# Kernel tuning notes

Hardware: AMD Instinct MI355X
Metric: run time of the kernel (lower is better)

Reference implementation:

```python
import jax, jax.numpy as jnp
import numpy as np

LAMBDA_LAME = 1.0
MU_LAME = 0.5
JACOBIAN_WEIGHT = 0.1
ERROR_BOUND = 0.01


def setup_inputs() -> dict:
    key = jax.random.key(0)
    df = jax.random.normal(key, (2, 3, 192, 192, 192), dtype=jnp.float32)
    return {"deformation_field": df}


def _grad(x, axis):
    # matches torch.gradient / np.gradient (edge_order=1): central diff in the
    # interior, one-sided first-order at the boundaries, unit spacing.
    return jnp.gradient(x, axis=axis)


def _robust(x, delta):
    abs_x = jnp.abs(x)
    return jnp.where(abs_x <= delta, 0.5 * x * x, delta * (abs_x - 0.5 * delta))


def reference(deformation_field):
    u = deformation_field[:, 0]  # [B, D, H, W]
    v = deformation_field[:, 1]
    w = deformation_field[:, 2]

    du_dx, du_dy, du_dz = _grad(u, 1), _grad(u, 2), _grad(u, 3)
    dv_dx, dv_dy, dv_dz = _grad(v, 1), _grad(v, 2), _grad(v, 3)
    dw_dx, dw_dy, dw_dz = _grad(w, 1), _grad(w, 2), _grad(w, 3)

    E_xx, E_yy, E_zz = du_dx, dv_dy, dw_dz
    E_xy = 0.5 * (du_dy + dv_dx)
    E_xz = 0.5 * (du_dz + dw_dx)
    E_yz = 0.5 * (dv_dz + dw_dy)
    trace_E = E_xx + E_yy + E_zz

    d = ERROR_BOUND
    tr_l = _robust(trace_E, d)
    energy = (0.5 * LAMBDA_LAME * tr_l ** 2
              + MU_LAME * (_robust(E_xx, d) ** 2 + _robust(E_yy, d) ** 2
                           + _robust(E_zz, d) ** 2
                           + 2.0 * (_robust(E_xy, d) ** 2
                                    + _robust(E_xz, d) ** 2
                                    + _robust(E_yz, d) ** 2)))

    jac = ((1 + du_dx) * ((1 + dv_dy) * (1 + dw_dz) - dv_dz * dw_dy)
           - du_dy * (dv_dx * (1 + dw_dz) - dv_dz * (1 + dw_dx))
           + du_dz * (dv_dx * dw_dy - (1 + dv_dy) * (1 + dw_dx)))
    jac_penalty = jax.nn.relu(-jac)

    total = jnp.mean(energy) + JACOBIAN_WEIGHT * jnp.mean(jac_penalty)
    return total
```

## Files before the change

kernel.cpp:

```cpp
#include <hip/hip_runtime.h>

#define DIM 192
#define PLANE (DIM * DIM)
#define VOL ((size_t)PLANE * DIM)
#define NTOT (2.0 * 14155776.0 / 2.0)

__device__ __forceinline__ float robustf(float x) {
    float ax = fabsf(x);
    return (ax <= 0.01f) ? (0.5f * x * x) : (0.01f * (ax - 0.005f));
}

__device__ __forceinline__ float4 ldg4(const float* __restrict__ p) {
    return *(const float4*)p;
}

__device__ __forceinline__ float voxel_loss(
    float du_dx, float du_dy, float du_dz,
    float dv_dx, float dv_dy, float dv_dz,
    float dw_dx, float dw_dy, float dw_dz) {
    const float E_xy = 0.5f * (du_dy + dv_dx);
    const float E_xz = 0.5f * (du_dz + dw_dx);
    const float E_yz = 0.5f * (dv_dz + dw_dy);
    const float tr   = du_dx + dv_dy + dw_dz;

    const float rtr = robustf(tr);
    const float rxx = robustf(du_dx), ryy = robustf(dv_dy), rzz = robustf(dw_dz);
    const float rxy = robustf(E_xy),  rxz = robustf(E_xz),  ryz = robustf(E_yz);

    const float energy = 0.5f * rtr * rtr
                       + 0.5f * (rxx * rxx + ryy * ryy + rzz * rzz
                                 + 2.0f * (rxy * rxy + rxz * rxz + ryz * ryz));

    const float jac =
          (1.0f + du_dx) * ((1.0f + dv_dy) * (1.0f + dw_dz) - dv_dz * dw_dy)
        - du_dy * (dv_dx * (1.0f + dw_dz) - dv_dz * (1.0f + dw_dx))
        + du_dz * (dv_dx * dw_dy - (1.0f + dv_dy) * (1.0f + dw_dx));

    return energy + 0.1f * fmaxf(-jac, 0.0f);
}

__device__ __forceinline__ float4 zgrad(float4 c, float lf, float rt,
                                        bool leftEdge, bool rightEdge) {
    float4 g;
    g.x = leftEdge  ? (c.y - c.x) : 0.5f * (c.y - lf);
    g.y = 0.5f * (c.z - c.x);
    g.z = 0.5f * (c.w - c.y);
    g.w = rightEdge ? (c.w - c.z) : 0.5f * (rt - c.z);
    return g;
}

__global__ __launch_bounds__(256)
void elastic_main(const float* __restrict__ df, double* __restrict__ acc) {
    const int tx = threadIdx.x;
    const int ty = threadIdx.y;
    const int k4 = tx * 4;
    const int j  = blockIdx.x * 4 + ty;
    const int i0 = blockIdx.y * 16;
    const int b  = blockIdx.z;

    const float* __restrict__ u = df + (size_t)(b * 3 + 0) * VOL;
    const float* __restrict__ v = df + (size_t)(b * 3 + 1) * VOL;
    const float* __restrict__ w = df + (size_t)(b * 3 + 2) * VOL;

    const int jp = (j < DIM - 1) ? j + 1 : j;
    const int jm = (j > 0) ? j - 1 : j;
    const float sy = ((jp - jm) == 2) ? 0.5f : 1.0f;

    const bool act = (tx < 48);
    const bool leftEdge  = (tx == 0);
    const bool rightEdge = (tx == 47);

    float vsum = 0.0f;

    for (int ii = 0; ii < 16; ++ii) {
        const int i = i0 + ii;
        const int ip = (i < DIM - 1) ? i + 1 : i;
        const int im = (i > 0) ? i - 1 : i;
        const float sx = ((ip - im) == 2) ? 0.5f : 1.0f;

        const size_t oC  = (size_t)i  * PLANE + (size_t)j  * DIM + k4;
        const size_t oXp = (size_t)ip * PLANE + (size_t)j  * DIM + k4;
        const size_t oXm = (size_t)im * PLANE + (size_t)j  * DIM + k4;
        const size_t oYp = (size_t)i  * PLANE + (size_t)jp * DIM + k4;
        const size_t oYm = (size_t)i  * PLANE + (size_t)jm * DIM + k4;

        float4 uc, vc, wc;
        float4 uxp, uxm, vxp, vxm, wxp, wxm;
        float4 uyp, uym, vyp, vym, wyp, wym;

        if (act) {
            uc  = ldg4(u + oC);  vc  = ldg4(v + oC);  wc  = ldg4(w + oC);
            uxp = ldg4(u + oXp); uxm = ldg4(u + oXm);
            vxp = ldg4(v + oXp); vxm = ldg4(v + oXm);
            wxp = ldg4(w + oXp); wxm = ldg4(w + oXm);
            uyp = ldg4(u + oYp); uym = ldg4(u + oYm);
            vyp = ldg4(v + oYp); vym = ldg4(v + oYm);
            wyp = ldg4(w + oYp); wym = ldg4(w + oYm);
        } else {
            uc = vc = wc = make_float4(0.f, 0.f, 0.f, 0.f);
        }

        const float ulf = __shfl_up(uc.w, 1);
        const float vlf = __shfl_up(vc.w, 1);
        const float wlf = __shfl_up(wc.w, 1);
        const float urt = __shfl_down(uc.x, 1);
        const float vrt = __shfl_down(vc.x, 1);
        const float wrt = __shfl_down(wc.x, 1);

        if (act) {
            const float4 du_dz = zgrad(uc, ulf, urt, leftEdge, rightEdge);
            const float4 dv_dz = zgrad(vc, vlf, vrt, leftEdge, rightEdge);
            const float4 dw_dz = zgrad(wc, wlf, wrt, leftEdge, rightEdge);

            float4 du_dx, dv_dx, dw_dx, du_dy, dv_dy, dw_dy;
            du_dx.x = (uxp.x - uxm.x) * sx; du_dx.y = (uxp.y - uxm.y) * sx;
            du_dx.z = (uxp.z - uxm.z) * sx; du_dx.w = (uxp.w - uxm.w) * sx;
            dv_dx.x = (vxp.x - vxm.x) * sx; dv_dx.y = (vxp.y - vxm.y) * sx;
            dv_dx.z = (vxp.z - vxm.z) * sx; dv_dx.w = (vxp.w - vxm.w) * sx;
            dw_dx.x = (wxp.x - wxm.x) * sx; dw_dx.y = (wxp.y - wxm.y) * sx;
            dw_dx.z = (wxp.z - wxm.z) * sx; dw_dx.w = (wxp.w - wxm.w) * sx;
            du_dy.x = (uyp.x - uym.x) * sy; du_dy.y = (uyp.y - uym.y) * sy;
            du_dy.z = (uyp.z - uym.z) * sy; du_dy.w = (uyp.w - uym.w) * sy;
            dv_dy.x = (vyp.x - vym.x) * sy; dv_dy.y = (vyp.y - vym.y) * sy;
            dv_dy.z = (vyp.z - vym.z) * sy; dv_dy.w = (vyp.w - vym.w) * sy;
            dw_dy.x = (wyp.x - wym.x) * sy; dw_dy.y = (wyp.y - wym.y) * sy;
            dw_dy.z = (wyp.z - wym.z) * sy; dw_dy.w = (wyp.w - wym.w) * sy;

            vsum += voxel_loss(du_dx.x, du_dy.x, du_dz.x,
                               dv_dx.x, dv_dy.x, dv_dz.x,
                               dw_dx.x, dw_dy.x, dw_dz.x);
            vsum += voxel_loss(du_dx.y, du_dy.y, du_dz.y,
                               dv_dx.y, dv_dy.y, dv_dz.y,
                               dw_dx.y, dw_dy.y, dw_dz.y);
            vsum += voxel_loss(du_dx.z, du_dy.z, du_dz.z,
                               dv_dx.z, dv_dy.z, dv_dz.z,
                               dw_dx.z, dw_dy.z, dw_dz.z);
            vsum += voxel_loss(du_dx.w, du_dy.w, du_dz.w,
                               dv_dx.w, dv_dy.w, dv_dz.w,
                               dw_dx.w, dw_dy.w, dw_dz.w);
        }
    }

    #pragma unroll
    for (int off = 32; off > 0; off >>= 1)
        vsum += __shfl_down(vsum, off, 64);

    __shared__ float wpart[4];
    if (tx == 0) wpart[ty] = vsum;
    __syncthreads();
    if (tx == 0 && ty == 0) {
        double s = (double)wpart[0] + (double)wpart[1]
                 + (double)wpart[2] + (double)wpart[3];
        unsafeAtomicAdd(acc, s);
    }
}

__global__ void elastic_finalize(const double* __restrict__ acc, float* __restrict__ out) {
    out[0] = (float)(acc[0] * (1.0 / 14155776.0));
}

extern "C" void kernel_launch(void* const* d_in, const int* in_sizes, int n_in,
                              void* d_out, int out_size, void* d_ws, size_t ws_size,
                              hipStream_t stream) {
    const float* df = (const float*)d_in[0];
    double* acc = (double*)d_ws;
    float* out = (float*)d_out;

    hipMemsetAsync(d_ws, 0, sizeof(double), stream);

    dim3 grid(48, 12, 2);
    dim3 block(64, 4);
    elastic_main<<<grid, block, 0, stream>>>(df, acc);
    elastic_finalize<<<1, 1, 0, stream>>>(acc, out);
}
```

Measured before the change: 261.4 us.

## Reuse x-neighbor planes via a rolling register window and lengthen the x-chunk

Each thread now keeps the previous and current x-planes of u, v and w in registers and rotates them every step. Per iteration it loads only the next x-plane plus the y-neighbours, cutting global/cache loads from 15 to 9 float4s. The x-chunk per block grows from 16 to 24 planes, which cuts the grid to 768 blocks, and a min-blocks hint is added to launch_bounds. The longer chunk amortises the warm-up loads but lowers the total number of resident waves, which may reduce latency hiding.

```diff
diff --git a/kernel.cpp b/kernel.cpp
--- a/kernel.cpp
+++ b/kernel.cpp
@@ -3,7 +3,6 @@
 #define DIM 192
 #define PLANE (DIM * DIM)
 #define VOL ((size_t)PLANE * DIM)
-#define NTOT (2.0 * 14155776.0 / 2.0)
 
 __device__ __forceinline__ float robustf(float x) {
     float ax = fabsf(x);
@@ -12,6 +11,11 @@
 
 __device__ __forceinline__ float4 ldg4(const float* __restrict__ p) {
     return *(const float4*)p;
+}
+
+__device__ __forceinline__ float4 sub_scale(float4 a, float4 b, float s) {
+    return make_float4((a.x - b.x) * s, (a.y - b.y) * s,
+                       (a.z - b.z) * s, (a.w - b.w) * s);
 }
 
 __device__ __forceinline__ float voxel_loss(
@@ -49,13 +53,13 @@
     return g;
 }
 
-__global__ __launch_bounds__(256)
+__global__ __launch_bounds__(256, 4)
 void elastic_main(const float* __restrict__ df, double* __restrict__ acc) {
     const int tx = threadIdx.x;
     const int ty = threadIdx.y;
     const int k4 = tx * 4;
     const int j  = blockIdx.x * 4 + ty;
-    const int i0 = blockIdx.y * 16;
+    const int i0 = blockIdx.y * 24;
     const int b  = blockIdx.z;
 
     const float* __restrict__ u = df + (size_t)(b * 3 + 0) * VOL;
@@ -70,34 +74,38 @@
     const bool leftEdge  = (tx == 0);
     const bool rightEdge = (tx == 47);
 
+    float4 um, vm, wm, uc, vc, wc;
+    um = vm = wm = uc = vc = wc = make_float4(0.f, 0.f, 0.f, 0.f);
+
+    {
+        const int im1 = (i0 > 0) ? i0 - 1 : 0;
+        const size_t oM = (size_t)im1 * PLANE + (size_t)j * DIM + k4;
+        const size_t oC = (size_t)i0  * PLANE + (size_t)j * DIM + k4;
+        if (act) {
+            um = ldg4(u + oM); vm = ldg4(v + oM); wm = ldg4(w + oM);
+            uc = ldg4(u + oC); vc = ldg4(v + oC); wc = ldg4(w + oC);
+        }
+    }
+
     float vsum = 0.0f;
 
-    for (int ii = 0; ii < 16; ++ii) {
-        const int i = i0 + ii;
-        const int ip = (i < DIM - 1) ? i + 1 : i;
-        const int im = (i > 0) ? i - 1 : i;
-        const float sx = ((ip - im) == 2) ? 0.5f : 1.0f;
+    for (int ii = 0; ii < 24; ++ii) {
+        const int i   = i0 + ii;
+        const int ip1 = (i < DIM - 1) ? i + 1 : i;
+        const int im1 = (i > 0) ? i - 1 : i;
+        const float sx = ((ip1 - im1) == 2) ? 0.5f : 1.0f;
 
-        const size_t oC  = (size_t)i  * PLANE + (size_t)j  * DIM + k4;
-        const size_t oXp = (size_t)ip * PLANE + (size_t)j  * DIM + k4;
-        const size_t oXm = (size_t)im * PLANE + (size_t)j  * DIM + k4;
-        const size_t oYp = (size_t)i  * PLANE + (size_t)jp * DIM + k4;
-        const size_t oYm = (size_t)i  * PLANE + (size_t)jm * DIM + k4;
+        const size_t oP  = (size_t)ip1 * PLANE + (size_t)j  * DIM + k4;
+        const size_t oYp = (size_t)i   * PLANE + (size_t)jp * DIM + k4;
+        const size_t oYm = (size_t)i   * PLANE + (size_t)jm * DIM + k4;
 
-        float4 uc, vc, wc;
-        float4 uxp, uxm, vxp, vxm, wxp, wxm;
-        float4 uyp, uym, vyp, vym, wyp, wym;
-
+        float4 up, vp, wp, uyp, uym, vyp, vym, wyp, wym;
+        up = vp = wp = make_float4(0.f, 0.f, 0.f, 0.f);
         if (act) {
-            uc  = ldg4(u + oC);  vc  = ldg4(v + oC);  wc  = ldg4(w + oC);
-            uxp = ldg4(u + oXp); uxm = ldg4(u + oXm);
-            vxp = ldg4(v + oXp); vxm = ldg4(v + oXm);
-            wxp = ldg4(w + oXp); wxm = ldg4(w + oXm);
+            up  = ldg4(u + oP);  vp  = ldg4(v + oP);  wp  = ldg4(w + oP);
             uyp = ldg4(u + oYp); uym = ldg4(u + oYm);
             vyp = ldg4(v + oYp); vym = ldg4(v + oYm);
             wyp = ldg4(w + oYp); wym = ldg4(w + oYm);
-        } else {
-            uc = vc = wc = make_float4(0.f, 0.f, 0.f, 0.f);
         }
 
         const float ulf = __shfl_up(uc.w, 1);
@@ -112,19 +120,12 @@
             const float4 dv_dz = zgrad(vc, vlf, vrt, leftEdge, rightEdge);
             const float4 dw_dz = zgrad(wc, wlf, wrt, leftEdge, rightEdge);
 
-            float4 du_dx, dv_dx, dw_dx, du_dy, dv_dy, dw_dy;
-            du_dx.x = (uxp.x - uxm.x) * sx; du_dx.y = (uxp.y - uxm.y) * sx;
-            du_dx.z = (uxp.z - uxm.z) * sx; du_dx.w = (uxp.w - uxm.w) * sx;
-            dv_dx.x = (vxp.x - vxm.x) * sx; dv_dx.y = (vxp.y - vxm.y) * sx;
-            dv_dx.z = (vxp.z - vxm.z) * sx; dv_dx.w = (vxp.w - vxm.w) * sx;
-            dw_dx.x = (wxp.x - wxm.x) * sx; dw_dx.y = (wxp.y - wxm.y) * sx;
-            dw_dx.z = (wxp.z - wxm.z) * sx; dw_dx.w = (wxp.w - wxm.w) * sx;
-            du_dy.x = (uyp.x - uym.x) * sy; du_dy.y = (uyp.y - uym.y) * sy;
-            du_dy.z = (uyp.z - uym.z) * sy; du_dy.w = (uyp.w - uym.w) * sy;
-            dv_dy.x = (vyp.x - vym.x) * sy; dv_dy.y = (vyp.y - vym.y) * sy;
-            dv_dy.z = (vyp.z - vym.z) * sy; dv_dy.w = (vyp.w - vym.w) * sy;
-            dw_dy.x = (wyp.x - wym.x) * sy; dw_dy.y = (wyp.y - wym.y) * sy;
-            dw_dy.z = (wyp.z - wym.z) * sy; dw_dy.w = (wyp.w - wym.w) * sy;
+            const float4 du_dx = sub_scale(up, um, sx);
+            const float4 dv_dx = sub_scale(vp, vm, sx);
+            const float4 dw_dx = sub_scale(wp, wm, sx);
+            const float4 du_dy = sub_scale(uyp, uym, sy);
+            const float4 dv_dy = sub_scale(vyp, vym, sy);
+            const float4 dw_dy = sub_scale(wyp, wym, sy);
 
             vsum += voxel_loss(du_dx.x, du_dy.x, du_dz.x,
                                dv_dx.x, dv_dy.x, dv_dz.x,
@@ -139,6 +140,9 @@
                                dv_dx.w, dv_dy.w, dv_dz.w,
                                dw_dx.w, dw_dy.w, dw_dz.w);
         }
+
+        um = uc; vm = vc; wm = wc;
+        uc = up; vc = vp; wc = wp;
     }
 
     #pragma unroll
@@ -168,7 +172,7 @@
 
     hipMemsetAsync(d_ws, 0, sizeof(double), stream);
 
-    dim3 grid(48, 12, 2);
+    dim3 grid(48, 8, 2);
     dim3 block(64, 4);
     elastic_main<<<grid, block, 0, stream>>>(df, acc);
     elastic_finalize<<<1, 1, 0, stream>>>(acc, out);
```

Result: faster. 254.5 us (-2.7%).
